# Kernel tuning notes

Measured on AMD Instinct MI355X. Metric: run time of the kernel, lower is better.

Reference implementation:

```python
import jax, jax.numpy as jnp
import numpy as np

D_IN = 2048
D_OUT = 2048
CTX = 2048
N_HEADS = 16
HEAD_DIM = D_OUT // N_HEADS
ROPE_BASE = 10000.0


def precompute_rope(head_dim, context_length, base=ROPE_BASE):
    inv_freq = 1.0 / (base ** (jnp.arange(0, head_dim, 2, dtype=jnp.float32) / head_dim))
    pos = jnp.arange(context_length, dtype=jnp.float32)
    angles = pos[:, None] * inv_freq[None, :]            # (ctx, head_dim/2)
    angles = jnp.concatenate([angles, angles], axis=-1)  # (ctx, head_dim)
    return jnp.cos(angles), jnp.sin(angles)


def compute_rope(x, cos, sin):
    # x: (b, h, s, d)
    s = x.shape[2]
    d = x.shape[3]
    x1, x2 = x[..., : d // 2], x[..., d // 2 :]
    rotated = jnp.concatenate([-x2, x1], axis=-1)
    c = cos[:s][None, None, :, :]
    sn = sin[:s][None, None, :, :]
    return x * c + rotated * sn


def setup_inputs() -> dict:
    key = jax.random.key(0)
    kx, kq, kk, kv, ko = jax.random.split(key, 5)
    scale = 1.0 / np.sqrt(D_IN)
    return {
        "x": jax.random.normal(kx, (2, 2048, D_IN), dtype=jnp.float32),
        "W_query": jax.random.normal(kq, (D_IN, D_OUT), dtype=jnp.float32) * scale,
        "W_key": jax.random.normal(kk, (D_IN, D_OUT), dtype=jnp.float32) * scale,
        "W_value": jax.random.normal(kv, (D_IN, D_OUT), dtype=jnp.float32) * scale,
        "W_out": jax.random.normal(ko, (D_OUT, D_OUT), dtype=jnp.float32) * scale,
    }


def reference(x, W_query, W_key, W_value, W_out):
    b, s, _ = x.shape
    cos, sin = precompute_rope(HEAD_DIM, CTX)

    def split_heads(t):
        return t.reshape(b, s, N_HEADS, HEAD_DIM).transpose(0, 2, 1, 3)  # (b,h,s,d)

    q = split_heads(x @ W_query)
    k = split_heads(x @ W_key)
    v = split_heads(x @ W_value)

    q = compute_rope(q, cos, sin)
    k = compute_rope(k, cos, sin)

    scores = jnp.einsum("bhqd,bhkd->bhqk", q, k) / jnp.sqrt(jnp.float32(HEAD_DIM))
    causal = jnp.tril(jnp.ones((s, s), dtype=bool))
    scores = jnp.where(causal[None, None], scores, -jnp.inf)
    attn = jax.nn.softmax(scores, axis=-1)

    ctx = jnp.einsum("bhqk,bhkd->bhqd", attn, v)
    ctx = ctx.transpose(0, 2, 1, 3).reshape(b, s, D_OUT)
    return ctx @ W_out
```

## Files before the change

### kernel.cpp

```cpp
#include <hip/hip_runtime.h>
#include <hip/hip_bf16.h>

typedef __attribute__((ext_vector_type(8))) short bf16x8;
typedef __attribute__((ext_vector_type(4))) float f32x4;
typedef __attribute__((ext_vector_type(16))) float f32x16;
typedef __attribute__((ext_vector_type(4))) unsigned int u32x4;

__device__ inline unsigned short f2bf(float f) {
    unsigned int u = __builtin_bit_cast(unsigned int, f);
    u += 0x7FFFu + ((u >> 16) & 1u);
    return (unsigned short)(u >> 16);
}
__device__ inline float bf2f(unsigned short h) {
    unsigned int u = ((unsigned int)h) << 16;
    return __builtin_bit_cast(float, u);
}
__device__ inline unsigned int pkbf(float a, float b) {
    return (unsigned int)f2bf(a) | ((unsigned int)f2bf(b) << 16);
}


__global__ void k_conv_x(const float* __restrict__ in, unsigned short* __restrict__ out, int n4) {
    int i = blockIdx.x * blockDim.x + threadIdx.x;
    if (i >= n4) return;
    float4 v = ((const float4*)in)[i];
    uint2 o;
    o.x = (unsigned)f2bf(v.x) | ((unsigned)f2bf(v.y) << 16);
    o.y = (unsigned)f2bf(v.z) | ((unsigned)f2bf(v.w) << 16);
    ((uint2*)out)[i] = o;
}

__global__ void k_wT(const float* __restrict__ w0, const float* __restrict__ w1,
                     const float* __restrict__ w2, const float* __restrict__ w3,
                     unsigned short* __restrict__ out) {
    __shared__ float tile[32][33];
    int z = blockIdx.z;
    const float* W = (z == 0) ? w0 : (z == 1) ? w1 : (z == 2) ? w2 : w3;
    unsigned short* O = out + (size_t)z * 2048 * 2048;
    int n0 = blockIdx.x * 32, k0 = blockIdx.y * 32;
    int tx = threadIdx.x & 31, ty = threadIdx.x >> 5;
#pragma unroll
    for (int j = 0; j < 4; ++j)
        tile[ty + j * 8][tx] = W[(size_t)(k0 + ty + j * 8) * 2048 + n0 + tx];
    __syncthreads();
#pragma unroll
    for (int j = 0; j < 4; ++j)
        O[(size_t)(n0 + ty + j * 8) * 2048 + k0 + tx] = f2bf(tile[tx][ty + j * 8]);
}

__global__ void k_rope_table(float* __restrict__ cosT, float* __restrict__ sinT) {
    int t = blockIdx.x * 256 + threadIdx.x;
    int s = t >> 6, i = t & 63;
    float inv = __expf(-((float)i / 64.0f) * 9.210340371976184f);
    float ang = (float)s * inv;
    cosT[t] = cosf(ang);
    sinT[t] = sinf(ang);
}

__global__ void k_rope_apply(unsigned short* qkv, const float* __restrict__ cosT,
                             const float* __restrict__ sinT) {
    int t = blockIdx.x * 256 + threadIdx.x;
    int i = t & 63, h = (t >> 6) & 15, s = (t >> 10) & 2047, b = t >> 21;
    float c = cosT[(s << 6) | i], sn = sinT[(s << 6) | i];
    size_t base = ((size_t)(b * 2048 + s)) * 2048 + h * 128 + i;
    const float SQ = 0.12751742f;
    {
        float a = bf2f(qkv[base]), bb = bf2f(qkv[base + 64]);
        qkv[base]      = f2bf((a * c - bb * sn) * SQ);
        qkv[base + 64] = f2bf((bb * c + a * sn) * SQ);
    }
    {
        size_t kbi = base + (size_t)8388608;
        float a = bf2f(qkv[kbi]), bb = bf2f(qkv[kbi + 64]);
        qkv[kbi]      = f2bf(a * c - bb * sn);
        qkv[kbi + 64] = f2bf(bb * c + a * sn);
    }
}

__global__ void k_vT(const unsigned short* __restrict__ V, unsigned short* __restrict__ VT) {
    __shared__ unsigned short tile[32][33];
    int z = blockIdx.z;
    int s0 = blockIdx.x * 32, d0 = blockIdx.y * 32;
    int b = z >> 4, h = z & 15;
    int tx = threadIdx.x & 31, ty = threadIdx.x >> 5;
#pragma unroll
    for (int j = 0; j < 4; ++j)
        tile[ty + j * 8][tx] =
            V[((size_t)(b * 2048 + s0 + ty + j * 8)) * 2048 + h * 128 + d0 + tx];
    __syncthreads();
#pragma unroll
    for (int j = 0; j < 4; ++j)
        VT[((size_t)(z * 128 + d0 + ty + j * 8)) * 2048 + s0 + tx] = tile[tx][ty + j * 8];
}

template <int OUT_MODE>
__global__ __launch_bounds__(256) void gemm_bt(const unsigned short* __restrict__ A,
                                               const unsigned short* __restrict__ Bt,
                                               void* __restrict__ outp, int M, int N, int K) {
    __shared__ __align__(16) unsigned short As[128 * 64];
    __shared__ __align__(16) unsigned short Bs[128 * 64];
    const int tid = threadIdx.x, w = tid >> 6, l = tid & 63;
    const int m0 = blockIdx.y * 128, n0 = blockIdx.x * 128;
    const int wm = w >> 1, wn = w & 1;
    const int l15 = l & 15, lq = l >> 4;
    f32x4 acc[4][4] = {};
    const int lr = l >> 3, lg = l & 7;
    const int srcg = lg ^ lr;

    const int nkt = K >> 6;
    for (int kt = 0; kt < nkt; ++kt) {
        if (kt) __syncthreads();
#pragma unroll
        for (int i = 0; i < 4; ++i) {
            int r0 = (w * 4 + i) * 8;
            int row = r0 + lr;
            const unsigned short* sa = A + (size_t)(m0 + row) * K + kt * 64 + srcg * 8;
            __builtin_amdgcn_global_load_lds((const void*)sa, (void*)&As[(w * 4 + i) * 512], 16, 0, 0);
            const unsigned short* sb = Bt + (size_t)(n0 + row) * K + kt * 64 + srcg * 8;
            __builtin_amdgcn_global_load_lds((const void*)sb, (void*)&Bs[(w * 4 + i) * 512], 16, 0, 0);
        }
        __syncthreads();
#pragma unroll
        for (int kb = 0; kb < 2; ++kb) {
            bf16x8 af[4], bfr[4];
#pragma unroll
            for (int mi = 0; mi < 4; ++mi) {
                int row = wm * 64 + mi * 16 + l15;
                int g = (kb * 4 + lq) ^ (row & 7);
                af[mi] = *(const bf16x8*)&As[row * 64 + g * 8];
            }
#pragma unroll
            for (int ni = 0; ni < 4; ++ni) {
                int row = wn * 64 + ni * 16 + l15;
                int g = (kb * 4 + lq) ^ (row & 7);
                bfr[ni] = *(const bf16x8*)&Bs[row * 64 + g * 8];
            }
#pragma unroll
            for (int mi = 0; mi < 4; ++mi)
#pragma unroll
                for (int ni = 0; ni < 4; ++ni)
                    acc[mi][ni] = __builtin_amdgcn_mfma_f32_16x16x32_bf16(af[mi], bfr[ni],
                                                                          acc[mi][ni], 0, 0, 0);
        }
    }

    if constexpr (OUT_MODE == 0) {
        int tsel = n0 >> 11, nloc = n0 & 2047;
        unsigned short* op = (unsigned short*)outp + (size_t)tsel * M * 2048;
#pragma unroll
        for (int mi = 0; mi < 4; ++mi)
#pragma unroll
            for (int ni = 0; ni < 4; ++ni)
#pragma unroll
                for (int r = 0; r < 4; ++r) {
                    int row = m0 + wm * 64 + mi * 16 + lq * 4 + r;
                    int col = nloc + wn * 64 + ni * 16 + l15;
                    op[(size_t)row * 2048 + col] = f2bf(acc[mi][ni][r]);
                }
    } else {
        float* op = (float*)outp;
#pragma unroll
        for (int mi = 0; mi < 4; ++mi)
#pragma unroll
            for (int ni = 0; ni < 4; ++ni)
#pragma unroll
                for (int r = 0; r < 4; ++r) {
                    int row = m0 + wm * 64 + mi * 16 + lq * 4 + r;
                    int col = n0 + wn * 64 + ni * 16 + l15;
                    op[(size_t)row * 2048 + col] = acc[mi][ni][r];
                }
    }
}

__global__ __launch_bounds__(256, 2) void k_attn(const unsigned short* __restrict__ Qp,
                                                 const unsigned short* __restrict__ Kp,
                                                 const unsigned short* __restrict__ VTp,
                                                 unsigned short* __restrict__ ctx) {
    __shared__ __align__(16) unsigned short Ks[2][64 * 128];
    __shared__ __align__(16) unsigned short Vs[2][128 * 64];
    const int tid = threadIdx.x, w = tid >> 6, l = tid & 63;
    const int l31 = l & 31, hi = l >> 5;
    const int x = blockIdx.x, bh = x & 31, pr = x >> 5;
    const int b = bh >> 4, h = bh & 15;
    const size_t b2048 = (size_t)b * 2048;
    const int h128 = h * 128;
    const size_t bh128 = (size_t)bh * 128;

    auto stage = [&](int kv) {
        const int bsel = kv & 1;
        const size_t kvoff = (size_t)kv * 64;
#pragma unroll
        for (int i = 0; i < 4; ++i) {
            int gi = w * 256 + i * 64 + l;
            int row = gi >> 4, g = gi & 15;
            int sg = g ^ (row & 7);
            const unsigned short* src = Kp + (b2048 + kvoff + row) * 2048 + h128 + sg * 8;
            __builtin_amdgcn_global_load_lds((const void*)src,
                                             (void*)&Ks[bsel][w * 2048 + i * 512], 16, 0, 0);
        }
#pragma unroll
        for (int i = 0; i < 4; ++i) {
            int gi = w * 256 + i * 64 + l;
            int row = gi >> 3, g = gi & 7;
            int sg = g ^ (row & 7);
            const unsigned short* src = VTp + (bh128 + row) * 2048 + kvoff + sg * 8;
            __builtin_amdgcn_global_load_lds((const void*)src,
                                             (void*)&Vs[bsel][w * 2048 + i * 512], 16, 0, 0);
        }
    };

    for (int pi = 0; pi < 2; ++pi) {
        const int t = pi ? pr : (15 - pr);
        const int q0 = t * 128;
        const int wrow0 = q0 + w * 32;
        const int qg = wrow0 + l31;

        bf16x8 qf[8];
        {
            const unsigned short* qb = Qp + (b2048 + qg) * 2048 + h128 + hi * 8;
#pragma unroll
            for (int ds = 0; ds < 8; ++ds) qf[ds] = *(const bf16x8*)(qb + ds * 16);
#pragma unroll
            for (int ds = 0; ds < 8; ++ds) asm volatile("" ::"v"(qf[ds]));
        }
        f32x16 Oa[4] = {};
        float m2 = -1e30f, l2 = 0.f;
        const int kvmax = 2 * t + 1;

        stage(0);
        for (int kv = 0; kv <= kvmax; ++kv) {
            const int cur = kv & 1;
            if (kv < kvmax) {
                stage(kv + 1);
                asm volatile("s_waitcnt vmcnt(8)" ::: "memory");
            } else {
                asm volatile("s_waitcnt vmcnt(0)" ::: "memory");
            }
            __builtin_amdgcn_s_barrier();
            __builtin_amdgcn_sched_barrier(0);

            const int kvb = kv * 64;
            if (kvb <= wrow0 + 31) {
                f32x16 S[2] = {};
                __builtin_amdgcn_s_setprio(1);
#pragma unroll
                for (int ds = 0; ds < 8; ++ds)
#pragma unroll
                    for (int st = 0; st < 2; ++st) {
                        int row = st * 32 + l31;
                        int g = (ds * 2 + hi) ^ (row & 7);
                        bf16x8 kf = *(const bf16x8*)&Ks[cur][row * 128 + g * 8];
                        S[st] = __builtin_amdgcn_mfma_f32_32x32x16_bf16(kf, qf[ds], S[st], 0, 0, 0);
                    }
                __builtin_amdgcn_s_setprio(0);

                if (kvb + 63 > wrow0) {
#pragma unroll
                    for (int st = 0; st < 2; ++st)
#pragma unroll
                        for (int r = 0; r < 16; ++r) {
                            int kpos = kvb + st * 32 + (r & 3) + 8 * (r >> 2) + 4 * hi;
                            if (kpos > qg) S[st][r] = -1e30f;
                        }
                }

                float pmax = -1e30f;
#pragma unroll
                for (int st = 0; st < 2; ++st)
#pragma unroll
                    for (int r = 0; r < 16; ++r) pmax = fmaxf(pmax, S[st][r]);
                pmax = fmaxf(pmax, __shfl_xor(pmax, 32));
                if (__any(pmax > m2 + 8.0f)) {
                    float mn = fmaxf(m2, pmax);
                    float sc = __builtin_amdgcn_exp2f(m2 - mn);
                    m2 = mn;
                    l2 *= sc;
#pragma unroll
                    for (int dt = 0; dt < 4; ++dt)
#pragma unroll
                        for (int e = 0; e < 16; ++e) Oa[dt][e] *= sc;
                }
                float rs = 0.f;
#pragma unroll
                for (int st = 0; st < 2; ++st)
#pragma unroll
                    for (int r = 0; r < 16; ++r) {
                        float p = __builtin_amdgcn_exp2f(S[st][r] - m2);
                        S[st][r] = p;
                        rs += p;
                    }
                rs += __shfl_xor(rs, 32);
                l2 += rs;

                bf16x8 pfrag[4];
#pragma unroll
                for (int ks = 0; ks < 4; ++ks) {
                    const int st = ks >> 1, base = (ks & 1) * 8;
                    unsigned int x0 = pkbf(S[st][base + 0], S[st][base + 1]);
                    unsigned int x1 = pkbf(S[st][base + 2], S[st][base + 3]);
                    unsigned int y0 = pkbf(S[st][base + 4], S[st][base + 5]);
                    unsigned int y1 = pkbf(S[st][base + 6], S[st][base + 7]);
                    unsigned int t0 = hi ? x0 : y0, t1 = hi ? x1 : y1;
                    t0 = (unsigned int)__shfl_xor((int)t0, 32);
                    t1 = (unsigned int)__shfl_xor((int)t1, 32);
                    u32x4 fw;
                    fw.x = hi ? t0 : x0;
                    fw.y = hi ? t1 : x1;
                    fw.z = hi ? y0 : t0;
                    fw.w = hi ? y1 : t1;
                    pfrag[ks] = __builtin_bit_cast(bf16x8, fw);
                }

                __builtin_amdgcn_s_setprio(1);
#pragma unroll
                for (int ks = 0; ks < 4; ++ks)
#pragma unroll
                    for (int dt = 0; dt < 4; ++dt) {
                        int row = dt * 32 + l31;
                        int g = (ks * 2 + hi) ^ (row & 7);
                        bf16x8 vf = *(const bf16x8*)&Vs[cur][row * 64 + g * 8];
                        Oa[dt] = __builtin_amdgcn_mfma_f32_32x32x16_bf16(vf, pfrag[ks], Oa[dt], 0, 0, 0);
                    }
                __builtin_amdgcn_s_setprio(0);
            }
            __builtin_amdgcn_sched_barrier(0);
            __builtin_amdgcn_s_barrier();
        }

        float inv = 1.0f / l2;
        unsigned short* cb = ctx + (b2048 + qg) * 2048 + h128;
#pragma unroll
        for (int dt = 0; dt < 4; ++dt)
#pragma unroll
            for (int g = 0; g < 4; ++g) {
                uint2 pv;
                pv.x = pkbf(Oa[dt][4 * g + 0] * inv, Oa[dt][4 * g + 1] * inv);
                pv.y = pkbf(Oa[dt][4 * g + 2] * inv, Oa[dt][4 * g + 3] * inv);
                *(uint2*)(cb + dt * 32 + 8 * g + 4 * hi) = pv;
            }
    }
}


extern "C" void kernel_launch(void* const* d_in, const int* in_sizes, int n_in,
                              void* d_out, int out_size, void* d_ws, size_t ws_size,
                              hipStream_t stream) {
    const float* x  = (const float*)d_in[0];
    const float* wq = (const float*)d_in[1];
    const float* wk = (const float*)d_in[2];
    const float* wv = (const float*)d_in[3];
    const float* wo = (const float*)d_in[4];

    char* ws = (char*)d_ws;
    unsigned short* xb  = (unsigned short*)(ws);
    unsigned short* wT  = (unsigned short*)(ws + 16777216);
    unsigned short* qkv = (unsigned short*)(ws + 50331648);
    unsigned short* vT  = (unsigned short*)(ws + 100663296);
    float* cosT = (float*)(ws + 117440512);
    float* sinT = (float*)(ws + 117964800);
    unsigned short* ctx = xb;

    k_conv_x<<<8192, 256, 0, stream>>>(x, xb, 2097152);
    k_wT<<<dim3(64, 64, 4), 256, 0, stream>>>(wq, wk, wv, wo, wT);
    k_rope_table<<<512, 256, 0, stream>>>(cosT, sinT);
    gemm_bt<0><<<dim3(48, 32), 256, 0, stream>>>(xb, wT, (void*)qkv, 4096, 6144, 2048);
    k_rope_apply<<<16384, 256, 0, stream>>>(qkv, cosT, sinT);
    k_vT<<<dim3(64, 4, 32), 256, 0, stream>>>(qkv + 2 * 8388608, vT);
    k_attn<<<256, 256, 0, stream>>>(qkv, qkv + 8388608, vT, ctx);
    gemm_bt<1><<<dim3(16, 32), 256, 0, stream>>>(ctx, wT + (size_t)3 * 4194304, d_out,
                                                 4096, 2048, 2048);
}
```

Baseline: 269.9 us.

## Double-buffer GEMM LDS tiles and widen block to 128x256 with 8 waves

Restructures the bf16 GEMM so the next K-tile is loaded into a second LDS buffer, using global_load_lds, while MFMAs run on the current one. Manual vmcnt waits and s_barrier calls replace the two __syncthreads per iteration. The block tile grows to 128x256 with 512 threads, so each A tile is reused across more columns. The cost is twice the LDS (96KB), which can lower occupancy, and the output GEMM now has only 256 blocks.

```diff
diff --git a/kernel.cpp b/kernel.cpp
--- a/kernel.cpp
+++ b/kernel.cpp
@@ -94,32 +94,52 @@
 }
 
 template <int OUT_MODE>
-__global__ __launch_bounds__(256) void gemm_bt(const unsigned short* __restrict__ A,
+__global__ __launch_bounds__(512) void gemm_bt(const unsigned short* __restrict__ A,
                                                const unsigned short* __restrict__ Bt,
                                                void* __restrict__ outp, int M, int N, int K) {
-    __shared__ __align__(16) unsigned short As[128 * 64];
-    __shared__ __align__(16) unsigned short Bs[128 * 64];
+    __shared__ __align__(16) unsigned short As[2][128 * 64];
+    __shared__ __align__(16) unsigned short Bs[2][256 * 64];
     const int tid = threadIdx.x, w = tid >> 6, l = tid & 63;
-    const int m0 = blockIdx.y * 128, n0 = blockIdx.x * 128;
-    const int wm = w >> 1, wn = w & 1;
+    const int m0 = blockIdx.y * 128, n0 = blockIdx.x * 256;
+    const int wm = w >> 2, wn = w & 3;
     const int l15 = l & 15, lq = l >> 4;
     f32x4 acc[4][4] = {};
-    const int lr = l >> 3, lg = l & 7;
-    const int srcg = lg ^ lr;
+
+    auto stage = [&](int kt, int bsel) {
+        const int kc = kt * 64;
+#pragma unroll
+        for (int i = 0; i < 2; ++i) {
+            int gi = (i * 8 + w) * 64 + l;
+            int row = gi >> 3, g = gi & 7;
+            int sg = g ^ (row & 7);
+            const unsigned short* src = A + (size_t)(m0 + row) * K + kc + sg * 8;
+            __builtin_amdgcn_global_load_lds((const void*)src,
+                                             (void*)&As[bsel][(i * 8 + w) * 512], 16, 0, 0);
+        }
+#pragma unroll
+        for (int i = 0; i < 4; ++i) {
+            int gi = (i * 8 + w) * 64 + l;
+            int row = gi >> 3, g = gi & 7;
+            int sg = g ^ (row & 7);
+            const unsigned short* src = Bt + (size_t)(n0 + row) * K + kc + sg * 8;
+            __builtin_amdgcn_global_load_lds((const void*)src,
+                                             (void*)&Bs[bsel][(i * 8 + w) * 512], 16, 0, 0);
+        }
+    };
 
     const int nkt = K >> 6;
+    stage(0, 0);
     for (int kt = 0; kt < nkt; ++kt) {
-        if (kt) __syncthreads();
-#pragma unroll
-        for (int i = 0; i < 4; ++i) {
-            int r0 = (w * 4 + i) * 8;
-            int row = r0 + lr;
-            const unsigned short* sa = A + (size_t)(m0 + row) * K + kt * 64 + srcg * 8;
-            __builtin_amdgcn_global_load_lds((const void*)sa, (void*)&As[(w * 4 + i) * 512], 16, 0, 0);
-            const unsigned short* sb = Bt + (size_t)(n0 + row) * K + kt * 64 + srcg * 8;
-            __builtin_amdgcn_global_load_lds((const void*)sb, (void*)&Bs[(w * 4 + i) * 512], 16, 0, 0);
-        }
-        __syncthreads();
+        const int cur = kt & 1;
+        if (kt + 1 < nkt) {
+            stage(kt + 1, cur ^ 1);
+            asm volatile("s_waitcnt vmcnt(6)" ::: "memory");
+        } else {
+            asm volatile("s_waitcnt vmcnt(0)" ::: "memory");
+        }
+        __builtin_amdgcn_s_barrier();
+        __builtin_amdgcn_sched_barrier(0);
+
 #pragma unroll
         for (int kb = 0; kb < 2; ++kb) {
             bf16x8 af[4], bfr[4];
@@ -127,13 +147,13 @@
             for (int mi = 0; mi < 4; ++mi) {
                 int row = wm * 64 + mi * 16 + l15;
                 int g = (kb * 4 + lq) ^ (row & 7);
-                af[mi] = *(const bf16x8*)&As[row * 64 + g * 8];
+                af[mi] = *(const bf16x8*)&As[cur][row * 64 + g * 8];
             }
 #pragma unroll
             for (int ni = 0; ni < 4; ++ni) {
                 int row = wn * 64 + ni * 16 + l15;
                 int g = (kb * 4 + lq) ^ (row & 7);
-                bfr[ni] = *(const bf16x8*)&Bs[row * 64 + g * 8];
+                bfr[ni] = *(const bf16x8*)&Bs[cur][row * 64 + g * 8];
             }
 #pragma unroll
             for (int mi = 0; mi < 4; ++mi)
@@ -142,6 +162,8 @@
                     acc[mi][ni] = __builtin_amdgcn_mfma_f32_16x16x32_bf16(af[mi], bfr[ni],
                                                                           acc[mi][ni], 0, 0, 0);
         }
+        __builtin_amdgcn_sched_barrier(0);
+        __builtin_amdgcn_s_barrier();
     }
 
     if constexpr (OUT_MODE == 0) {
@@ -363,10 +385,10 @@
     k_conv_x<<<8192, 256, 0, stream>>>(x, xb, 2097152);
     k_wT<<<dim3(64, 64, 4), 256, 0, stream>>>(wq, wk, wv, wo, wT);
     k_rope_table<<<512, 256, 0, stream>>>(cosT, sinT);
-    gemm_bt<0><<<dim3(48, 32), 256, 0, stream>>>(xb, wT, (void*)qkv, 4096, 6144, 2048);
+    gemm_bt<0><<<dim3(24, 32), 512, 0, stream>>>(xb, wT, (void*)qkv, 4096, 6144, 2048);
     k_rope_apply<<<16384, 256, 0, stream>>>(qkv, cosT, sinT);
     k_vT<<<dim3(64, 4, 32), 256, 0, stream>>>(qkv + 2 * 8388608, vT);
     k_attn<<<256, 256, 0, stream>>>(qkv, qkv + 8388608, vT, ctx);
-    gemm_bt<1><<<dim3(16, 32), 256, 0, stream>>>(ctx, wT + (size_t)3 * 4194304, d_out,
-                                                 4096, 2048, 2048);
-}
+    gemm_bt<1><<<dim3(8, 32), 512, 0, stream>>>(ctx, wT + (size_t)3 * 4194304, d_out,
+                                                4096, 2048, 2048);
+}
```

Measured after the change: 309.3 us. +14.6%, slower.
